# Optimization experiments

Measured on AMD Instinct MI355X. Metric: run time of the kernel, lower is better.

## Reference

```python
import jax, jax.numpy as jnp
import numpy as np

N_NODES = 50000
N_EDGES = 800000
C = 4      # num_channels
F_IN = 64
F_OUT = 64


def setup_inputs() -> dict:
    key = jax.random.key(0)
    k0, k1, k2, k3 = jax.random.split(key, 4)
    x = jax.random.normal(k0, (N_NODES, C, F_IN), dtype=jnp.float32)
    edge_index = jax.random.randint(k1, (2, N_EDGES), 0, N_NODES, dtype=jnp.int64)
    edge_weight = jax.random.uniform(k2, (N_EDGES,), dtype=jnp.float32)
    # per-channel GCNConv weights (glorot-ish) and biases
    W = jax.random.normal(k3, (C, F_IN, F_OUT), dtype=jnp.float32) / jnp.sqrt(jnp.float32(F_IN))
    b = jnp.zeros((C, F_OUT), dtype=jnp.float32)
    return {"x": x, "edge_index": edge_index, "edge_weight": edge_weight, "W": W, "b": b}


def reference(x, edge_index, edge_weight, W, b):
    # Batched-over-channels GCNConv (normalize=True, add_self_loops=True):
    # out[:, c, :] = D^{-1/2} (A + I) D^{-1/2} (x[:, c, :] @ W[c]) + b[c]
    n = x.shape[0]
    loop = jnp.arange(n, dtype=edge_index.dtype)
    row = jnp.concatenate([edge_index[0], loop])   # source
    col = jnp.concatenate([edge_index[1], loop])   # target
    ew = jnp.concatenate([edge_weight, jnp.ones((n,), dtype=edge_weight.dtype)])
    deg = jax.ops.segment_sum(ew, col, num_segments=n)
    dinv = jnp.where(deg > 0, jax.lax.rsqrt(deg), jnp.zeros_like(deg))
    norm = dinv[row] * ew * dinv[col]              # [E+N]
    xw = jnp.einsum('ncf,cfo->nco', x, W)          # per-channel linear transform
    msgs = xw[row] * norm[:, None, None]           # gather + scale, [E+N, C, F_OUT]
    out = jax.ops.segment_sum(msgs, col, num_segments=n)  # scatter-add
    return out + b[None, :, :]
```

## Files before the change

kernel.cpp:

```cpp
#include <hip/hip_runtime.h>

#define C_CH 4
#define F_INN 64
#define F_OUTT 64
#define CF 256
#define SCAN_TILE 1024
#define FIXP 33554432.0f
#define XSP 68

static __device__ __forceinline__ unsigned rne16(float f) {
    unsigned u = __float_as_uint(f);
    return (u + 0x7fffu + ((u >> 16) & 1u)) >> 16;
}
static __device__ __forceinline__ unsigned pk2(float a, float b) {
    return rne16(a) | (rne16(b) << 16);
}

__global__ __launch_bounds__(256) void histxw_kernel(
        const int* __restrict__ col, const float* __restrict__ ew,
        unsigned long long* __restrict__ cd64, int* __restrict__ rank, int E,
        const float* __restrict__ x, const float* __restrict__ W,
        unsigned* __restrict__ xwb, int n) {
    __shared__ float xs[64][XSP];
    __shared__ float ws[64][64];
    int t = threadIdx.x;
    int bid = blockIdx.x;

    int e = bid * 256 + t;
    bool has = (e < E);
    unsigned long long old = 0;
    if (has) {
        int d = col[e];
        unsigned fx = __float2uint_rn(ew[e] * FIXP);
        old = atomicAdd(&cd64[d], (1ULL << 32) | (unsigned long long)fx);
    }

    int c = bid & 3;
    int N0 = (bid >> 2) * 64;
    {
        const float4* Wc4 = reinterpret_cast<const float4*>(W + (size_t)c * F_INN * F_OUTT);
        float4* ws4 = reinterpret_cast<float4*>(&ws[0][0]);
#pragma unroll
        for (int r = 0; r < 4; ++r) ws4[t + 256 * r] = Wc4[t + 256 * r];
    }
    {
        int r = t >> 2;
        int node = N0 + r;
        int kq = (t & 3) * 4;
        const float* __restrict__ xrow = x + (size_t)node * CF + c * F_INN;
#pragma unroll
        for (int rep = 0; rep < 4; ++rep) {
            int k = kq + rep * 16;
            float4 v = (node < n) ? *reinterpret_cast<const float4*>(xrow + k)
                                  : make_float4(0.f, 0.f, 0.f, 0.f);
            xs[k + 0][r] = v.x;
            xs[k + 1][r] = v.y;
            xs[k + 2][r] = v.z;
            xs[k + 3][r] = v.w;
        }
    }
    __syncthreads();

    int fi = t & 15;
    int ni = t >> 4;
    float acc[4][4];
#pragma unroll
    for (int j = 0; j < 4; ++j)
#pragma unroll
        for (int o = 0; o < 4; ++o) acc[j][o] = 0.f;

#pragma unroll 8
    for (int k = 0; k < F_INN; ++k) {
        float4 a = *reinterpret_cast<const float4*>(&xs[k][4 * ni]);
        float4 b = *reinterpret_cast<const float4*>(&ws[k][4 * fi]);
        float av[4] = {a.x, a.y, a.z, a.w};
        float bv[4] = {b.x, b.y, b.z, b.w};
#pragma unroll
        for (int j = 0; j < 4; ++j)
#pragma unroll
            for (int o = 0; o < 4; ++o) acc[j][o] = fmaf(av[j], bv[o], acc[j][o]);
    }

#pragma unroll
    for (int j = 0; j < 4; ++j) {
        int node = N0 + 4 * ni + j;
        if (node < n) {
            uint2 pkd;
            pkd.x = pk2(acc[j][0], acc[j][1]);
            pkd.y = pk2(acc[j][2], acc[j][3]);
            size_t eidx = (size_t)node * CF + c * F_OUTT + 4 * fi;
            *reinterpret_cast<uint2*>(xwb + (eidx >> 1)) = pkd;
        }
    }

    if (has) rank[e] = (int)(old >> 32);
}

__global__ __launch_bounds__(SCAN_TILE) void scan1_kernel(
        const unsigned long long* __restrict__ cd64,
        int* __restrict__ offs, int* __restrict__ blk, int n) {
    __shared__ int s[SCAN_TILE];
    int t = threadIdx.x;
    int g = blockIdx.x * SCAN_TILE + t;
    int v = (g < n) ? (int)(cd64[g] >> 32) : 0;
    s[t] = v;
    __syncthreads();
    for (int d = 1; d < SCAN_TILE; d <<= 1) {
        int x = (t >= d) ? s[t - d] : 0;
        __syncthreads();
        s[t] += x;
        __syncthreads();
    }
    if (g < n) offs[g] = s[t] - v;
    if (t == SCAN_TILE - 1) blk[blockIdx.x] = s[t];
}

__global__ __launch_bounds__(256) void scan23_kernel(int* __restrict__ offs,
                                                     const int* __restrict__ blk,
                                                     const unsigned long long* __restrict__ cd64,
                                                     float* __restrict__ dinv, int n, int nb) {
    __shared__ int sI[64];
    __shared__ int sE[64];
    int t = threadIdx.x;
    int v = 0;
    if (t < 64) {
        v = (t < nb) ? blk[t] : 0;
        sI[t] = v;
    }
    __syncthreads();
    for (int d = 1; d < 64; d <<= 1) {
        int x = (t < 64 && t >= d) ? sI[t - d] : 0;
        __syncthreads();
        if (t < 64) sI[t] += x;
        __syncthreads();
    }
    if (t < 64) sE[t] = sI[t] - v;
    __syncthreads();

    int g = blockIdx.x * 256 + t;
    if (g < n) {
        offs[g] += sE[g >> 10];
        float deg = 1.0f + (float)(unsigned)(cd64[g] & 0xffffffffULL) * (1.0f / FIXP);
        dinv[g] = rsqrtf(deg);
    }
    if (g == 0) offs[n] = sI[nb - 1];
}

__global__ void scatter_kernel(const int* __restrict__ row, const int* __restrict__ col,
                               const float* __restrict__ ew, const float* __restrict__ dinv,
                               const int* __restrict__ offs, const int* __restrict__ rank,
                               int2* __restrict__ edata, int E) {
    int e = blockIdx.x * blockDim.x + threadIdx.x;
    if (e < E) {
        int r = row[e];
        int d = col[e];
        float nrm = dinv[r] * ew[e] * dinv[d];
        edata[offs[d] + rank[e]] = make_int2(r, __float_as_int(nrm));
    }
}

__global__ __launch_bounds__(256) void gather_kernel(const int* __restrict__ offs,
                                                     const int2* __restrict__ edata,
                                                     const float* __restrict__ dinv,
                                                     const unsigned* __restrict__ xwb,
                                                     const float* __restrict__ b,
                                                     float* __restrict__ out, int n) {
    int v = (int)((blockIdx.x * 256u + threadIdx.x) >> 6);
    int lane = threadIdx.x & 63;
    if (v >= n) return;

    int beg = offs[v];
    int end = offs[v + 1];
    float di = dinv[v];
    float s = di * di;

    const uint2* __restrict__ xw2 = reinterpret_cast<const uint2*>(xwb);
    uint2 uself = xw2[(size_t)v * 64 + lane];
    const float4 bv = *reinterpret_cast<const float4*>(b + lane * 4);
    float4 acc;
    acc.x = fmaf(__uint_as_float(uself.x << 16), s, bv.x);
    acc.y = fmaf(__uint_as_float(uself.x & 0xffff0000u), s, bv.y);
    acc.z = fmaf(__uint_as_float(uself.y << 16), s, bv.z);
    acc.w = fmaf(__uint_as_float(uself.y & 0xffff0000u), s, bv.w);

    int j = beg;
    int e4 = beg + ((end - beg) & ~3);
    for (; j < e4; j += 4) {
        int2 e0 = edata[j + 0];
        int2 e1 = edata[j + 1];
        int2 e2 = edata[j + 2];
        int2 e3 = edata[j + 3];
        uint2 u0 = xw2[(size_t)e0.x * 64 + lane];
        uint2 u1 = xw2[(size_t)e1.x * 64 + lane];
        uint2 u2 = xw2[(size_t)e2.x * 64 + lane];
        uint2 u3 = xw2[(size_t)e3.x * 64 + lane];
        float n0 = __int_as_float(e0.y), n1 = __int_as_float(e1.y);
        float n2 = __int_as_float(e2.y), n3 = __int_as_float(e3.y);
        acc.x = fmaf(__uint_as_float(u0.x << 16), n0, acc.x);
        acc.y = fmaf(__uint_as_float(u0.x & 0xffff0000u), n0, acc.y);
        acc.z = fmaf(__uint_as_float(u0.y << 16), n0, acc.z);
        acc.w = fmaf(__uint_as_float(u0.y & 0xffff0000u), n0, acc.w);
        acc.x = fmaf(__uint_as_float(u1.x << 16), n1, acc.x);
        acc.y = fmaf(__uint_as_float(u1.x & 0xffff0000u), n1, acc.y);
        acc.z = fmaf(__uint_as_float(u1.y << 16), n1, acc.z);
        acc.w = fmaf(__uint_as_float(u1.y & 0xffff0000u), n1, acc.w);
        acc.x = fmaf(__uint_as_float(u2.x << 16), n2, acc.x);
        acc.y = fmaf(__uint_as_float(u2.x & 0xffff0000u), n2, acc.y);
        acc.z = fmaf(__uint_as_float(u2.y << 16), n2, acc.z);
        acc.w = fmaf(__uint_as_float(u2.y & 0xffff0000u), n2, acc.w);
        acc.x = fmaf(__uint_as_float(u3.x << 16), n3, acc.x);
        acc.y = fmaf(__uint_as_float(u3.x & 0xffff0000u), n3, acc.y);
        acc.z = fmaf(__uint_as_float(u3.y << 16), n3, acc.z);
        acc.w = fmaf(__uint_as_float(u3.y & 0xffff0000u), n3, acc.w);
    }
    for (; j < end; ++j) {
        int2 ed = edata[j];
        float nrm = __int_as_float(ed.y);
        uint2 u0 = xw2[(size_t)ed.x * 64 + lane];
        acc.x = fmaf(__uint_as_float(u0.x << 16), nrm, acc.x);
        acc.y = fmaf(__uint_as_float(u0.x & 0xffff0000u), nrm, acc.y);
        acc.z = fmaf(__uint_as_float(u0.y << 16), nrm, acc.z);
        acc.w = fmaf(__uint_as_float(u0.y & 0xffff0000u), nrm, acc.w);
    }
    *reinterpret_cast<float4*>(out + (size_t)v * CF + lane * 4) = acc;
}

extern "C" void kernel_launch(void* const* d_in, const int* in_sizes, int n_in,
                              void* d_out, int out_size, void* d_ws, size_t ws_size,
                              hipStream_t stream) {
    const float* x  = (const float*)d_in[0];
    const int*   ei = (const int*)d_in[1];
    const float* ew = (const float*)d_in[2];
    const float* W  = (const float*)d_in[3];
    const float* b  = (const float*)d_in[4];
    float* out = (float*)d_out;

    int n = in_sizes[0] / (C_CH * F_INN);
    int E = in_sizes[2];

    const int* row = ei;
    const int* col = ei + E;

    auto align_up = [](size_t v) { return (v + 255) & ~(size_t)255; };
    char* p = (char*)d_ws;
    unsigned long long* cd64 = (unsigned long long*)p;  p += align_up((size_t)n * 8);
    int*   rank = (int*)p;                   p += align_up((size_t)E * 4);
    int*   offs = (int*)p;                   p += align_up(((size_t)n + 1) * 4);
    int*   blk  = (int*)p;                   p += align_up(64 * 4);
    float* dinv = (float*)p;                 p += align_up((size_t)n * 4);
    int2*  edata= (int2*)p;                  p += align_up((size_t)E * 8);
    unsigned* xwb = (unsigned*)p;

    int nb = (n + SCAN_TILE - 1) / SCAN_TILE;
    int nbFused = ((n + 63) / 64) * C_CH;

    hipMemsetAsync(cd64, 0, (size_t)n * 8, stream);
    histxw_kernel<<<nbFused, 256, 0, stream>>>(col, ew, cd64, rank, E, x, W, xwb, n);
    scan1_kernel<<<nb, SCAN_TILE, 0, stream>>>(cd64, offs, blk, n);
    scan23_kernel<<<(n + 255) / 256, 256, 0, stream>>>(offs, blk, cd64, dinv, n, nb);
    scatter_kernel<<<(E + 255) / 256, 256, 0, stream>>>(row, col, ew, dinv, offs, rank, edata, E);
    gather_kernel<<<(n * 64 + 255) / 256, 256, 0, stream>>>(offs, edata, dinv, xwb, b, out, n);
}
```

Before: 145.5 us.

## Use wavefront shuffle scans, 2 edges per scatter thread, 8-way gather unroll

```diff
diff --git a/kernel.cpp b/kernel.cpp
--- a/kernel.cpp
+++ b/kernel.cpp
@@ -99,42 +99,55 @@
 __global__ __launch_bounds__(SCAN_TILE) void scan1_kernel(
         const unsigned long long* __restrict__ cd64,
         int* __restrict__ offs, int* __restrict__ blk, int n) {
-    __shared__ int s[SCAN_TILE];
+    __shared__ int wsum[16];
     int t = threadIdx.x;
+    int lane = t & 63;
+    int wid = t >> 6;
     int g = blockIdx.x * SCAN_TILE + t;
     int v = (g < n) ? (int)(cd64[g] >> 32) : 0;
-    s[t] = v;
-    __syncthreads();
-    for (int d = 1; d < SCAN_TILE; d <<= 1) {
-        int x = (t >= d) ? s[t - d] : 0;
-        __syncthreads();
-        s[t] += x;
-        __syncthreads();
-    }
-    if (g < n) offs[g] = s[t] - v;
-    if (t == SCAN_TILE - 1) blk[blockIdx.x] = s[t];
+
+    int s = v;
+#pragma unroll
+    for (int d = 1; d < 64; d <<= 1) {
+        int u = __shfl_up(s, d);
+        if (lane >= d) s += u;
+    }
+    if (lane == 63) wsum[wid] = s;
+    __syncthreads();
+    if (wid == 0 && lane < 16) {
+        int w = wsum[lane];
+        int ws = w;
+#pragma unroll
+        for (int d = 1; d < 16; d <<= 1) {
+            int u = __shfl_up(ws, d);
+            if (lane >= d) ws += u;
+        }
+        wsum[lane] = ws - w;
+    }
+    __syncthreads();
+    int incl = s + wsum[wid];
+    if (g < n) offs[g] = incl - v;
+    if (t == SCAN_TILE - 1) blk[blockIdx.x] = incl;
 }
 
 __global__ __launch_bounds__(256) void scan23_kernel(int* __restrict__ offs,
                                                      const int* __restrict__ blk,
                                                      const unsigned long long* __restrict__ cd64,
                                                      float* __restrict__ dinv, int n, int nb) {
-    __shared__ int sI[64];
     __shared__ int sE[64];
+    __shared__ int sTot;
     int t = threadIdx.x;
-    int v = 0;
     if (t < 64) {
-        v = (t < nb) ? blk[t] : 0;
-        sI[t] = v;
-    }
-    __syncthreads();
-    for (int d = 1; d < 64; d <<= 1) {
-        int x = (t < 64 && t >= d) ? sI[t - d] : 0;
-        __syncthreads();
-        if (t < 64) sI[t] += x;
-        __syncthreads();
-    }
-    if (t < 64) sE[t] = sI[t] - v;
+        int v = (t < nb) ? blk[t] : 0;
+        int s = v;
+#pragma unroll
+        for (int d = 1; d < 64; d <<= 1) {
+            int u = __shfl_up(s, d);
+            if (t >= d) s += u;
+        }
+        sE[t] = s - v;
+        if (t == 63) sTot = s;
+    }
     __syncthreads();
 
     int g = blockIdx.x * 256 + t;
@@ -143,19 +156,23 @@
         float deg = 1.0f + (float)(unsigned)(cd64[g] & 0xffffffffULL) * (1.0f / FIXP);
         dinv[g] = rsqrtf(deg);
     }
-    if (g == 0) offs[n] = sI[nb - 1];
+    if (g == 0) offs[n] = sTot;
 }
 
 __global__ void scatter_kernel(const int* __restrict__ row, const int* __restrict__ col,
                                const float* __restrict__ ew, const float* __restrict__ dinv,
                                const int* __restrict__ offs, const int* __restrict__ rank,
                                int2* __restrict__ edata, int E) {
-    int e = blockIdx.x * blockDim.x + threadIdx.x;
-    if (e < E) {
-        int r = row[e];
-        int d = col[e];
-        float nrm = dinv[r] * ew[e] * dinv[d];
-        edata[offs[d] + rank[e]] = make_int2(r, __float_as_int(nrm));
+    int base = blockIdx.x * 512 + threadIdx.x;
+#pragma unroll
+    for (int q = 0; q < 2; ++q) {
+        int e = base + q * 256;
+        if (e < E) {
+            int r = row[e];
+            int d = col[e];
+            float nrm = dinv[r] * ew[e] * dinv[d];
+            edata[offs[d] + rank[e]] = make_int2(r, __float_as_int(nrm));
+        }
     }
 }
 
@@ -184,34 +201,39 @@
     acc.w = fmaf(__uint_as_float(uself.y & 0xffff0000u), s, bv.w);
 
     int j = beg;
-    int e4 = beg + ((end - beg) & ~3);
+    int e8 = beg + ((end - beg) & ~7);
+    for (; j < e8; j += 8) {
+        int2 ee[8];
+        uint2 uu[8];
+#pragma unroll
+        for (int q = 0; q < 8; ++q) ee[q] = edata[j + q];
+#pragma unroll
+        for (int q = 0; q < 8; ++q) uu[q] = xw2[(size_t)ee[q].x * 64 + lane];
+#pragma unroll
+        for (int q = 0; q < 8; ++q) {
+            float nn = __int_as_float(ee[q].y);
+            acc.x = fmaf(__uint_as_float(uu[q].x << 16), nn, acc.x);
+            acc.y = fmaf(__uint_as_float(uu[q].x & 0xffff0000u), nn, acc.y);
+            acc.z = fmaf(__uint_as_float(uu[q].y << 16), nn, acc.z);
+            acc.w = fmaf(__uint_as_float(uu[q].y & 0xffff0000u), nn, acc.w);
+        }
+    }
+    int e4 = j + ((end - j) & ~3);
     for (; j < e4; j += 4) {
-        int2 e0 = edata[j + 0];
-        int2 e1 = edata[j + 1];
-        int2 e2 = edata[j + 2];
-        int2 e3 = edata[j + 3];
-        uint2 u0 = xw2[(size_t)e0.x * 64 + lane];
-        uint2 u1 = xw2[(size_t)e1.x * 64 + lane];
-        uint2 u2 = xw2[(size_t)e2.x * 64 + lane];
-        uint2 u3 = xw2[(size_t)e3.x * 64 + lane];
-        float n0 = __int_as_float(e0.y), n1 = __int_as_float(e1.y);
-        float n2 = __int_as_float(e2.y), n3 = __int_as_float(e3.y);
-        acc.x = fmaf(__uint_as_float(u0.x << 16), n0, acc.x);
-        acc.y = fmaf(__uint_as_float(u0.x & 0xffff0000u), n0, acc.y);
-        acc.z = fmaf(__uint_as_float(u0.y << 16), n0, acc.z);
-        acc.w = fmaf(__uint_as_float(u0.y & 0xffff0000u), n0, acc.w);
-        acc.x = fmaf(__uint_as_float(u1.x << 16), n1, acc.x);
-        acc.y = fmaf(__uint_as_float(u1.x & 0xffff0000u), n1, acc.y);
-        acc.z = fmaf(__uint_as_float(u1.y << 16), n1, acc.z);
-        acc.w = fmaf(__uint_as_float(u1.y & 0xffff0000u), n1, acc.w);
-        acc.x = fmaf(__uint_as_float(u2.x << 16), n2, acc.x);
-        acc.y = fmaf(__uint_as_float(u2.x & 0xffff0000u), n2, acc.y);
-        acc.z = fmaf(__uint_as_float(u2.y << 16), n2, acc.z);
-        acc.w = fmaf(__uint_as_float(u2.y & 0xffff0000u), n2, acc.w);
-        acc.x = fmaf(__uint_as_float(u3.x << 16), n3, acc.x);
-        acc.y = fmaf(__uint_as_float(u3.x & 0xffff0000u), n3, acc.y);
-        acc.z = fmaf(__uint_as_float(u3.y << 16), n3, acc.z);
-        acc.w = fmaf(__uint_as_float(u3.y & 0xffff0000u), n3, acc.w);
+        int2 ee[4];
+        uint2 uu[4];
+#pragma unroll
+        for (int q = 0; q < 4; ++q) ee[q] = edata[j + q];
+#pragma unroll
+        for (int q = 0; q < 4; ++q) uu[q] = xw2[(size_t)ee[q].x * 64 + lane];
+#pragma unroll
+        for (int q = 0; q < 4; ++q) {
+            float nn = __int_as_float(ee[q].y);
+            acc.x = fmaf(__uint_as_float(uu[q].x << 16), nn, acc.x);
+            acc.y = fmaf(__uint_as_float(uu[q].x & 0xffff0000u), nn, acc.y);
+            acc.z = fmaf(__uint_as_float(uu[q].y << 16), nn, acc.z);
+            acc.w = fmaf(__uint_as_float(uu[q].y & 0xffff0000u), nn, acc.w);
+        }
     }
     for (; j < end; ++j) {
         int2 ed = edata[j];
@@ -258,6 +280,6 @@
     histxw_kernel<<<nbFused, 256, 0, stream>>>(col, ew, cd64, rank, E, x, W, xwb, n);
     scan1_kernel<<<nb, SCAN_TILE, 0, stream>>>(cd64, offs, blk, n);
     scan23_kernel<<<(n + 255) / 256, 256, 0, stream>>>(offs, blk, cd64, dinv, n, nb);
-    scatter_kernel<<<(E + 255) / 256, 256, 0, stream>>>(row, col, ew, dinv, offs, rank, edata, E);
+    scatter_kernel<<<(E + 511) / 512, 256, 0, stream>>>(row, col, ew, dinv, offs, rank, edata, E);
     gather_kernel<<<(n * 64 + 255) / 256, 256, 0, stream>>>(offs, edata, dinv, xwb, b, out, n);
 }
```

Result: no change. 145.2 us (-0.2%).
